# Kernel tuning notes

Hardware: AMD Instinct MI355X
Metric: run time of the kernel (lower is better)

The kernel has to match this reference:

```python
import jax, jax.numpy as jnp
import numpy as np

EPS = 1e-6      # l2_norm / denom clamp eps
BN_EPS = 1e-5   # BatchNorm eps


def _l2norm(x):
    # torch.norm(p=2, dim=-2, keepdim=True).clamp_min(eps)
    n = jnp.sqrt(jnp.sum(x * x, axis=-2, keepdims=True))
    return x / jnp.maximum(n, EPS)


def setup_inputs() -> dict:
    key = jax.random.key(0)
    ks = jax.random.split(key, 9)
    B, Cin_each, Co, H, W = 4, 256, 256, 128, 128
    Cq = Co // 8  # in_places // scale
    Cin = 4 * Cin_each
    return {
        "s5": jax.random.normal(ks[0], (B, Cin_each, H, W), jnp.float32),
        "s4": jax.random.normal(ks[1], (B, Cin_each, H, W), jnp.float32),
        "s3": jax.random.normal(ks[2], (B, Cin_each, H, W), jnp.float32),
        "s2": jax.random.normal(ks[3], (B, Cin_each, H, W), jnp.float32),
        # ConvBnRelu: 1x1 conv (no bias) + BN affine params
        "w_conv": jax.random.normal(ks[4], (Co, Cin), jnp.float32) * 0.03,
        "bn_gamma": jnp.ones((Co,), jnp.float32),
        "bn_beta": jnp.zeros((Co,), jnp.float32),
        # Attention 1x1 convs (with bias)
        "wq": jax.random.normal(ks[5], (Cq, Co), jnp.float32) * 0.06,
        "bq": jnp.zeros((Cq,), jnp.float32),
        "wk": jax.random.normal(ks[6], (Cq, Co), jnp.float32) * 0.06,
        "bk": jnp.zeros((Cq,), jnp.float32),
        "wv": jax.random.normal(ks[7], (Co, Co), jnp.float32) * 0.06,
        "bv": jnp.zeros((Co,), jnp.float32),
        # gamma is Parameter(zeros(1)) in the source; set nonzero so the
        # attention branch contributes to the output for kernel testing.
        "gamma": jnp.array(0.5, jnp.float32),
    }


def reference(s5, s4, s3, s2, w_conv, bn_gamma, bn_beta,
              wq, bq, wk, bk, wv, bv, gamma):
    # --- ConvBnRelu (1x1 conv, train-mode BN, ReLU) ---
    fcat = jnp.concatenate([s5, s4, s3, s2], axis=1)            # [B, 4C, H, W]
    x = jnp.einsum('oc,bchw->bohw', w_conv, fcat)               # 1x1 conv
    mu = x.mean(axis=(0, 2, 3), keepdims=True)
    var = x.var(axis=(0, 2, 3), keepdims=True)                  # biased, as torch BN
    x = (x - mu) / jnp.sqrt(var + BN_EPS)
    x = x * bn_gamma[None, :, None, None] + bn_beta[None, :, None, None]
    feat = jax.nn.relu(x)                                       # [B, C, H, W]

    # --- linear Attention (L2-norm QK, KV trick, no softmax) ---
    B, C, H, W = feat.shape
    N = H * W
    X = feat.reshape(B, C, N)
    Q = jnp.einsum('qc,bcn->bqn', wq, X) + bq[None, :, None]    # [B, Cq, N]
    K = jnp.einsum('qc,bcn->bqn', wk, X) + bk[None, :, None]    # [B, Cq, N]
    V = jnp.einsum('oc,bcn->bon', wv, X) + bv[None, :, None]    # [B, C, N]

    Qn = _l2norm(Q)                                             # norm over channel dim
    Kn = _l2norm(K)

    # denom: N + Q . sum_n K
    e = jnp.einsum('bqn,bq->bn', Qn, Kn.sum(axis=-1))           # [B, N]
    tailor = 1.0 / jnp.maximum(jnp.asarray(N, Qn.dtype) + e, 1e-6)

    # KV trick: [B, Cq, C] then project back through Q
    matrix = jnp.einsum('bqn,bcn->bqc', Kn, V)                  # [B, Cq, C]
    matrix_sum = V.sum(axis=-1)[:, :, None] + \
        jnp.einsum('bqn,bqc->bcn', Qn, matrix)                  # [B, C, N]

    weight_value = matrix_sum * tailor[:, None, :]              # [B, C, N]
    out = gamma * weight_value.reshape(B, C, H, W)
    out = jnp.nan_to_num(out, nan=0.0, posinf=1.0, neginf=-1.0)

    return out + feat
```

## Files before the change

### kernel.cpp

```cpp
#include <hip/hip_runtime.h>

#define B_   4
#define CO   256
#define CIN  1024
#define CQ   32
#define HN   16384
#define NPIX 65536
#define NTOT ((size_t)B_ * CO * HN)

typedef unsigned short ushort_t;
typedef __attribute__((ext_vector_type(8))) short bf16x8;
typedef __attribute__((ext_vector_type(4))) float f32x4;

__device__ __forceinline__ unsigned bf16pair(float x, float y) {
    unsigned xu = __float_as_uint(x), yu = __float_as_uint(y);
    unsigned xr = (xu + 0x7FFFu + ((xu >> 16) & 1u)) >> 16;
    unsigned yr = (yu + 0x7FFFu + ((yu >> 16) & 1u)) >> 16;
    return xr | (yr << 16);
}
__device__ __forceinline__ ushort_t bf16of(float x) {
    unsigned u = __float_as_uint(x);
    return (ushort_t)((u + 0x7FFFu + ((u >> 16) & 1u)) >> 16);
}
__device__ __forceinline__ float bf2f(ushort_t h) {
    return __uint_as_float(((unsigned)h) << 16);
}
__device__ __forceinline__ void unpack8(uint4 u, float* f) {
    f[0] = __uint_as_float(u.x << 16); f[1] = __uint_as_float(u.x & 0xffff0000u);
    f[2] = __uint_as_float(u.y << 16); f[3] = __uint_as_float(u.y & 0xffff0000u);
    f[4] = __uint_as_float(u.z << 16); f[5] = __uint_as_float(u.z & 0xffff0000u);
    f[6] = __uint_as_float(u.w << 16); f[7] = __uint_as_float(u.w & 0xffff0000u);
}
__device__ __forceinline__ void async16(void* lds, const void* g) {
    __builtin_amdgcn_global_load_lds(
        (const __attribute__((address_space(1))) void*)g,
        (__attribute__((address_space(3))) void*)lds, 16, 0, 0);
}

__global__ __launch_bounds__(256) void wcvt(
    const float* __restrict__ w, const float* __restrict__ wq,
    const float* __restrict__ wk, const float* __restrict__ wv,
    ushort_t* __restrict__ w_bf, ushort_t* __restrict__ wqk_bf,
    ushort_t* __restrict__ wv_bf)
{
    int i = blockIdx.x * 256 + threadIdx.x;
    if (i < 262144) {
        w_bf[i] = bf16of(w[i]);
    } else if (i < 278528) {
        int l = i - 262144; int row = l >> 8, col = l & 255;
        float v = (row < 32) ? wq[row * 256 + col] : wk[(row - 32) * 256 + col];
        wqk_bf[l] = bf16of(v);
    } else {
        int l = i - 278528;
        wv_bf[l] = bf16of(wv[l]);
    }
}

__global__ __launch_bounds__(256) void conv_mfma4(
    const float* __restrict__ s5, const float* __restrict__ s4,
    const float* __restrict__ s3, const float* __restrict__ s2,
    const ushort_t* __restrict__ w_bf, ushort_t* __restrict__ xb,
    float* __restrict__ accum)
{
    __shared__ ushort_t Aw[2][128 * 32];
    __shared__ ushort_t Bn[2][128 * 40];
    const int o0 = blockIdx.x * 128;
    const int n0 = blockIdx.y * 128;
    const int b  = blockIdx.z;
    const int tid = threadIdx.x;
    const int wave = tid >> 6, lane = tid & 63, l15 = lane & 15, quad = lane >> 4;
    const int wm = wave & 1, wn = wave >> 1;
    const int n_st = tid & 127;
    const int kqb  = tid >> 7;
    const int bswz = ((n_st >> 3) & 3) << 1;
    f32x4 acc[4][4] = {};
    float v[4][4];

    auto loadB = [&](int k0) {
        const float* base = (k0 < 256) ? s5 : (k0 < 512) ? s4
                          : (k0 < 768) ? s3 : s2;
        const float* sp = base + ((size_t)b * 256 + (k0 & 255)) * HN + n0 + n_st;
        #pragma unroll
        for (int i = 0; i < 4; ++i) {
            const float* cp = sp + (size_t)(kqb + 2 * i) * 4 * HN;
            #pragma unroll
            for (int j = 0; j < 4; ++j) v[i][j] = cp[(size_t)j * HN];
        }
    };
    auto storeB = [&](int bi) {
        ushort_t* Bp = Bn[bi];
        #pragma unroll
        for (int i = 0; i < 4; ++i) {
            int pos = (kqb + 2 * i) ^ bswz;
            uint2 u = make_uint2(bf16pair(v[i][0], v[i][1]),
                                 bf16pair(v[i][2], v[i][3]));
            *(uint2*)&Bp[n_st * 40 + pos * 4] = u;
        }
    };
    auto issueA = [&](int k0, int bi) {
        #pragma unroll
        for (int r = 0; r < 2; ++r) {
            int row  = r * 64 + wave * 16;
            int orow = row + (lane >> 2);
            const ushort_t* g = w_bf + (size_t)(o0 + orow) * CIN + k0
                                + (((lane & 3) ^ ((orow >> 1) & 3)) << 3);
            async16(&Aw[bi][row * 32], g);
        }
    };

    issueA(0, 0);
    loadB(0);

    int buf = 0;
    for (int k0 = 0; k0 < CIN; k0 += 32) {
        storeB(buf);
        asm volatile("s_waitcnt lgkmcnt(0)" ::: "memory");
        __builtin_amdgcn_s_barrier();
        __builtin_amdgcn_sched_barrier(0);
        if (k0 + 32 < CIN) { issueA(k0 + 32, buf ^ 1); loadB(k0 + 32); }
        bf16x8 af[4], bfv[4];
        #pragma unroll
        for (int tm = 0; tm < 4; ++tm) {
            int orow = wm * 64 + tm * 16 + l15;
            int pos  = quad ^ ((orow >> 1) & 3);
            af[tm] = *(const bf16x8*)&Aw[buf][orow * 32 + pos * 8];
        }
        #pragma unroll
        for (int tn = 0; tn < 4; ++tn) {
            int nl = wn * 64 + tn * 16 + l15;
            int p0 = (2 * quad) ^ (((nl >> 3) & 3) << 1);
            bfv[tn] = *(const bf16x8*)&Bn[buf][nl * 40 + p0 * 4];
        }
        #pragma unroll
        for (int tm = 0; tm < 4; ++tm)
            #pragma unroll
            for (int tn = 0; tn < 4; ++tn)
                acc[tm][tn] = __builtin_amdgcn_mfma_f32_16x16x32_bf16(
                    af[tm], bfv[tn], acc[tm][tn], 0, 0, 0);
        buf ^= 1;
    }

    #pragma unroll
    for (int tm = 0; tm < 4; ++tm)
        #pragma unroll
        for (int r = 0; r < 4; ++r) {
            float s = 0.f, ss = 0.f;
            #pragma unroll
            for (int tn = 0; tn < 4; ++tn) {
                float x = acc[tm][tn][r];
                s += x; ss += x * x;
            }
            s += __shfl_xor(s, 1); ss += __shfl_xor(ss, 1);
            s += __shfl_xor(s, 2); ss += __shfl_xor(ss, 2);
            s += __shfl_xor(s, 4); ss += __shfl_xor(ss, 4);
            s += __shfl_xor(s, 8); ss += __shfl_xor(ss, 8);
            if (l15 == 0) {
                int o = o0 + wm * 64 + tm * 16 + quad * 4 + r;
                atomicAdd(&accum[o], s);
                atomicAdd(&accum[256 + o], ss);
            }
        }

    ushort_t* st = Bn[0];
    const int orow = tid >> 3, oseg = tid & 7;
    #pragma unroll
    for (int tm = 0; tm < 4; ++tm) {
        if (tm) __syncthreads();
        #pragma unroll
        for (int r = 0; r < 4; ++r) {
            int row = wm * 16 + quad * 4 + r;
            #pragma unroll
            for (int tn = 0; tn < 4; ++tn)
                st[row * 136 + wn * 64 + tn * 16 + l15] = bf16of(acc[tm][tn][r]);
        }
        __syncthreads();
        {
            int c = o0 + (orow >> 4) * 64 + tm * 16 + (orow & 15);
            size_t base = ((size_t)(b * CO + c)) * HN + n0 + oseg * 16;
            const uint4* sp = (const uint4*)&st[orow * 136 + oseg * 16];
            *(uint4*)(xb + base)     = sp[0];
            *(uint4*)(xb + base + 8) = sp[1];
        }
    }
}

__global__ __launch_bounds__(256) void bn_finalize(
    const float* __restrict__ accum, const float* __restrict__ g,
    const float* __restrict__ bt, float* __restrict__ scale,
    float* __restrict__ shift)
{
    int o = threadIdx.x;
    float mu  = accum[o] / (float)NPIX;
    float var = accum[256 + o] / (float)NPIX - mu * mu;
    float sc  = g[o] * rsqrtf(var + 1e-5f);
    scale[o] = sc;
    shift[o] = bt[o] - mu * sc;
}

__global__ __launch_bounds__(256) void bnrelu_t(
    const ushort_t* __restrict__ xb, const float* __restrict__ scale,
    const float* __restrict__ shift, ushort_t* __restrict__ featT)
{
    __shared__ ushort_t sh[64 * 68];
    const int hn0 = blockIdx.x * 64, c0 = blockIdx.y * 64, b = blockIdx.z;
    const int tid = threadIdx.x;
    {
        int cl = tid >> 2, seg = tid & 3;
        float sc = scale[c0 + cl], sf = shift[c0 + cl];
        const ushort_t* src = xb + ((size_t)(b * CO + c0 + cl)) * HN + hn0 + seg * 16;
        #pragma unroll
        for (int h = 0; h < 2; ++h) {
            uint4 u = *(const uint4*)(src + h * 8);
            float f[8]; unpack8(u, f);
            #pragma unroll
            for (int j = 0; j < 8; ++j) {
                float v = fmaxf(fmaf(sc, f[j], sf), 0.f);
                sh[(seg * 16 + h * 8 + j) * 68 + cl] = bf16of(v);
            }
        }
    }
    __syncthreads();
    {
        int nl = tid >> 2, seg = tid & 3;
        size_t gn = (size_t)b * HN + hn0 + nl;
        ushort_t* dst = featT + gn * CO + c0 + seg * 16;
        #pragma unroll
        for (int j = 0; j < 4; ++j)
            *(uint2*)(dst + j * 4) = *(const uint2*)&sh[nl * 68 + seg * 16 + j * 4];
    }
}

__global__ __launch_bounds__(256) void qk_mfma(
    const ushort_t* __restrict__ featT, const ushort_t* __restrict__ wqk_bf,
    const float* __restrict__ bq, const float* __restrict__ bk,
    ushort_t* __restrict__ Qt, ushort_t* __restrict__ KtT,
    float* __restrict__ Ksum)
{
    __shared__ ushort_t At[128 * 32];
    __shared__ ushort_t Bt[64 * 32];
    const int n0 = blockIdx.x * 128;
    const int b  = n0 >> 14;
    const int hn0 = n0 & 16383;
    const int tid = threadIdx.x;
    const int wave = tid >> 6, lane = tid & 63, l15 = lane & 15, quad = lane >> 4;
    const int nsub = (wave & 1) * 64;
    const int isK  = wave >> 1;
    f32x4 acc[4][2] = {};

    for (int k0 = 0; k0 < CO; k0 += 32) {
        #pragma unroll
        for (int r = 0; r < 2; ++r) {
            int row = r * 64 + wave * 16;
            const ushort_t* g = featT + (size_t)(n0 + row + (lane >> 2)) * CO
                                + k0 + (lane & 3) * 8;
            async16(&At[row * 32], g);
        }
        {
            int row = wave * 16;
            const ushort_t* g = wqk_bf + (size_t)(row + (lane >> 2)) * CO
                                + k0 + (lane & 3) * 8;
            async16(&Bt[row * 32], g);
        }
        __syncthreads();
        bf16x8 af[4], bfv[2];
        #pragma unroll
        for (int tm = 0; tm < 4; ++tm)
            af[tm] = *(const bf16x8*)&At[(nsub + tm * 16 + l15) * 32 + quad * 8];
        #pragma unroll
        for (int tc = 0; tc < 2; ++tc)
            bfv[tc] = *(const bf16x8*)&Bt[(isK * 32 + tc * 16 + l15) * 32 + quad * 8];
        #pragma unroll
        for (int tm = 0; tm < 4; ++tm)
            #pragma unroll
            for (int tc = 0; tc < 2; ++tc)
                acc[tm][tc] = __builtin_amdgcn_mfma_f32_16x16x32_bf16(
                    af[tm], bfv[tc], acc[tm][tc], 0, 0, 0);
        __syncthreads();
    }
    const float bias0 = isK ? bk[l15]      : bq[l15];
    const float bias1 = isK ? bk[16 + l15] : bq[16 + l15];
    float ks0 = 0.f, ks1 = 0.f;
    #pragma unroll
    for (int tm = 0; tm < 4; ++tm)
        #pragma unroll
        for (int r = 0; r < 4; ++r) {
            float v0 = acc[tm][0][r] + bias0;
            float v1 = acc[tm][1][r] + bias1;
            float sq = v0 * v0 + v1 * v1;
            sq += __shfl_xor(sq, 1); sq += __shfl_xor(sq, 2);
            sq += __shfl_xor(sq, 4); sq += __shfl_xor(sq, 8);
            float inv = 1.f / fmaxf(sqrtf(sq), 1e-6f);
            v0 *= inv; v1 *= inv;
            if (isK) {
                int hn = hn0 + nsub + tm * 16 + quad * 4 + r;
                KtT[((size_t)(b * CQ + l15)) * HN + hn]      = bf16of(v0);
                KtT[((size_t)(b * CQ + 16 + l15)) * HN + hn] = bf16of(v1);
            } else {
                int n = n0 + nsub + tm * 16 + quad * 4 + r;
                Qt[(size_t)n * CQ + l15]      = bf16of(v0);
                Qt[(size_t)n * CQ + 16 + l15] = bf16of(v1);
            }
            ks0 += v0; ks1 += v1;
        }
    if (isK) {
        ks0 += __shfl_xor(ks0, 16); ks0 += __shfl_xor(ks0, 32);
        ks1 += __shfl_xor(ks1, 16); ks1 += __shfl_xor(ks1, 32);
        if (quad == 0) {
            atomicAdd(&Ksum[b * CQ + l15],      ks0);
            atomicAdd(&Ksum[b * CQ + 16 + l15], ks1);
        }
    }
}

__global__ __launch_bounds__(256) void v_kv_mfma(
    const ushort_t* __restrict__ featT, const ushort_t* __restrict__ wv_bf,
    const float* __restrict__ bv, const ushort_t* __restrict__ KtT,
    float* __restrict__ matT, float* __restrict__ Vsum)
{
    __shared__ ushort_t sh[128 * 136];
    ushort_t* At = sh;
    ushort_t* Bt = sh + 4096;
    const int n0  = blockIdx.x * 128;
    const int co0 = blockIdx.y * 128;
    const int b   = n0 >> 14;
    const int hn0 = n0 & 16383;
    const int tid = threadIdx.x;
    const int wave = tid >> 6, lane = tid & 63, l15 = lane & 15, quad = lane >> 4;
    const int wm = wave & 1, wn = wave >> 1;
    f32x4 acc[4][4] = {};

    for (int k0 = 0; k0 < CO; k0 += 32) {
        #pragma unroll
        for (int r = 0; r < 2; ++r) {
            int row = r * 64 + wave * 16;
            const ushort_t* ga = featT + (size_t)(n0 + row + (lane >> 2)) * CO
                                 + k0 + (lane & 3) * 8;
            async16(&At[row * 32], ga);
            const ushort_t* gb = wv_bf + (size_t)(co0 + row + (lane >> 2)) * CO
                                 + k0 + (lane & 3) * 8;
            async16(&Bt[row * 32], gb);
        }
        __syncthreads();
        bf16x8 af[4], bfv[4];
        #pragma unroll
        for (int tm = 0; tm < 4; ++tm)
            af[tm] = *(const bf16x8*)&At[(wm * 64 + tm * 16 + l15) * 32 + quad * 8];
        #pragma unroll
        for (int tn = 0; tn < 4; ++tn)
            bfv[tn] = *(const bf16x8*)&Bt[(wn * 64 + tn * 16 + l15) * 32 + quad * 8];
        #pragma unroll
        for (int tm = 0; tm < 4; ++tm)
            #pragma unroll
            for (int tn = 0; tn < 4; ++tn)
                acc[tm][tn] = __builtin_amdgcn_mfma_f32_16x16x32_bf16(
                    af[tm], bfv[tn], acc[tm][tn], 0, 0, 0);
        __syncthreads();
    }
    ushort_t* Vlds = sh;
    float bvl[4], vsum_p[4] = {};
    #pragma unroll
    for (int tn = 0; tn < 4; ++tn) bvl[tn] = bv[co0 + wn * 64 + tn * 16 + l15];
    #pragma unroll
    for (int tm = 0; tm < 4; ++tm)
        #pragma unroll
        for (int tn = 0; tn < 4; ++tn) {
            float x0 = acc[tm][tn][0] + bvl[tn];
            float x1 = acc[tm][tn][1] + bvl[tn];
            float x2 = acc[tm][tn][2] + bvl[tn];
            float x3 = acc[tm][tn][3] + bvl[tn];
            vsum_p[tn] += (x0 + x1) + (x2 + x3);
            uint2 u = make_uint2(bf16pair(x0, x1), bf16pair(x2, x3));
            int c_loc = wn * 64 + tn * 16 + l15;
            int nb    = wm * 64 + tm * 16 + quad * 4;
            *(uint2*)&Vlds[c_loc * 136 + nb] = u;
        }
    #pragma unroll
    for (int tn = 0; tn < 4; ++tn) {
        float s = vsum_p[tn];
        s += __shfl_xor(s, 16); s += __shfl_xor(s, 32);
        if (quad == 0)
            atomicAdd(&Vsum[b * CO + co0 + wn * 64 + tn * 16 + l15], s);
    }
    __syncthreads();
    f32x4 acc2[2][2] = {};
    #pragma unroll
    for (int ks = 0; ks < 4; ++ks) {
        bf16x8 a2[2], b2[2];
        #pragma unroll
        for (int t2 = 0; t2 < 2; ++t2)
            a2[t2] = *(const bf16x8*)&Vlds[(wave * 32 + t2 * 16 + l15) * 136
                                           + ks * 32 + quad * 8];
        #pragma unroll
        for (int tc = 0; tc < 2; ++tc)
            b2[tc] = *(const bf16x8*)&KtT[((size_t)(b * CQ + tc * 16 + l15)) * HN
                                          + hn0 + ks * 32 + quad * 8];
        #pragma unroll
        for (int t2 = 0; t2 < 2; ++t2)
            #pragma unroll
            for (int tc = 0; tc < 2; ++tc)
                acc2[t2][tc] = __builtin_amdgcn_mfma_f32_16x16x32_bf16(
                    a2[t2], b2[tc], acc2[t2][tc], 0, 0, 0);
    }
    #pragma unroll
    for (int t2 = 0; t2 < 2; ++t2)
        #pragma unroll
        for (int tc = 0; tc < 2; ++tc)
            #pragma unroll
            for (int r = 0; r < 4; ++r) {
                int c = co0 + wave * 32 + t2 * 16 + quad * 4 + r;
                atomicAdd(&matT[b * 8192 + c * CQ + tc * 16 + l15],
                          acc2[t2][tc][r]);
            }
}

__global__ __launch_bounds__(256) void tailor_k(
    const ushort_t* __restrict__ Qt, const float* __restrict__ Ksum,
    float* __restrict__ tailor)
{
    __shared__ float ks[CQ];
    const int n = blockIdx.x * 256 + threadIdx.x;
    const int b = n >> 14;
    if (threadIdx.x < CQ) ks[threadIdx.x] = Ksum[b * CQ + threadIdx.x];
    __syncthreads();
    const uint4* q = (const uint4*)&Qt[(size_t)n * CQ];
    float e = 0.f;
    #pragma unroll
    for (int i = 0; i < 4; ++i) {
        float f[8]; unpack8(q[i], f);
        #pragma unroll
        for (int j = 0; j < 8; ++j) e += f[j] * ks[i * 8 + j];
    }
    tailor[n] = 1.f / fmaxf((float)HN + e, 1e-6f);
}

__global__ __launch_bounds__(256) void final_mfma(
    const ushort_t* __restrict__ xb, const ushort_t* __restrict__ Qt,
    const float* __restrict__ matT, const float* __restrict__ Vsum,
    const float* __restrict__ tailor, const float* __restrict__ scale,
    const float* __restrict__ shift, const float* __restrict__ gamma_p,
    float* __restrict__ out)
{
    __shared__ float sh[32 * 132];
    const int c0 = blockIdx.x * 128;
    const int n0 = blockIdx.y * 128;
    const int b  = n0 >> 14, hn0 = n0 & 16383;
    const int tid = threadIdx.x;
    const int wave = tid >> 6, lane = tid & 63, l15 = lane & 15, quad = lane >> 4;
    const int wm = wave & 1, wn = wave >> 1;
    const float gamma = gamma_p[0];

    bf16x8 af[4], bfv[4];
    #pragma unroll
    for (int tm = 0; tm < 4; ++tm) {
        int c = c0 + wm * 64 + tm * 16 + l15;
        const float* mp = matT + b * 8192 + c * CQ + quad * 8;
        float4 m0 = *(const float4*)mp;
        float4 m1 = *(const float4*)(mp + 4);
        union { bf16x8 v; unsigned u[4]; } t;
        t.u[0] = bf16pair(m0.x, m0.y); t.u[1] = bf16pair(m0.z, m0.w);
        t.u[2] = bf16pair(m1.x, m1.y); t.u[3] = bf16pair(m1.z, m1.w);
        af[tm] = t.v;
    }
    #pragma unroll
    for (int tn = 0; tn < 4; ++tn) {
        int n = n0 + wn * 64 + tn * 16 + l15;
        bfv[tn] = *(const bf16x8*)&Qt[(size_t)n * CQ + quad * 8];
    }
    f32x4 acc[4][4] = {};
    #pragma unroll
    for (int tm = 0; tm < 4; ++tm)
        #pragma unroll
        for (int tn = 0; tn < 4; ++tn)
            acc[tm][tn] = __builtin_amdgcn_mfma_f32_16x16x32_bf16(
                af[tm], bfv[tn], acc[tm][tn], 0, 0, 0);

    float tl[4];
    #pragma unroll
    for (int tn = 0; tn < 4; ++tn) tl[tn] = tailor[n0 + wn * 64 + tn * 16 + l15];

    const int orow = tid >> 3, oseg = tid & 7;
    #pragma unroll
    for (int tm = 0; tm < 4; ++tm) {
        if (tm) __syncthreads();
        #pragma unroll
        for (int r = 0; r < 4; ++r) {
            int c = c0 + wm * 64 + tm * 16 + quad * 4 + r;
            float vs = Vsum[b * CO + c];
            int row = wm * 16 + quad * 4 + r;
            #pragma unroll
            for (int tn = 0; tn < 4; ++tn) {
                float val = gamma * (acc[tm][tn][r] + vs) * tl[tn];
                if (isnan(val)) val = 0.f;
                else if (isinf(val)) val = (val > 0.f) ? 1.f : -1.f;
                sh[row * 132 + wn * 64 + tn * 16 + l15] = val;
            }
        }
        __syncthreads();
        {
            int c = c0 + (orow >> 4) * 64 + tm * 16 + (orow & 15);
            float sc = scale[c], sf = shift[c];
            size_t base = ((size_t)(b * CO + c)) * HN + hn0 + oseg * 16;
            const float* sp = &sh[orow * 132 + oseg * 16];
            const uint4* xp = (const uint4*)(xb + base);
            #pragma unroll
            for (int h = 0; h < 2; ++h) {
                uint4 u = xp[h];
                float f[8]; unpack8(u, f);
                float4 q0, q1;
                q0.x = sp[h * 8 + 0] + fmaxf(fmaf(sc, f[0], sf), 0.f);
                q0.y = sp[h * 8 + 1] + fmaxf(fmaf(sc, f[1], sf), 0.f);
                q0.z = sp[h * 8 + 2] + fmaxf(fmaf(sc, f[2], sf), 0.f);
                q0.w = sp[h * 8 + 3] + fmaxf(fmaf(sc, f[3], sf), 0.f);
                q1.x = sp[h * 8 + 4] + fmaxf(fmaf(sc, f[4], sf), 0.f);
                q1.y = sp[h * 8 + 5] + fmaxf(fmaf(sc, f[5], sf), 0.f);
                q1.z = sp[h * 8 + 6] + fmaxf(fmaf(sc, f[6], sf), 0.f);
                q1.w = sp[h * 8 + 7] + fmaxf(fmaf(sc, f[7], sf), 0.f);
                *(float4*)(out + base + h * 8)     = q0;
                *(float4*)(out + base + h * 8 + 4) = q1;
            }
        }
    }
}

extern "C" void kernel_launch(void* const* d_in, const int* in_sizes, int n_in,
                              void* d_out, int out_size, void* d_ws, size_t ws_size,
                              hipStream_t stream)
{
    const float* s5      = (const float*)d_in[0];
    const float* s4      = (const float*)d_in[1];
    const float* s3      = (const float*)d_in[2];
    const float* s2      = (const float*)d_in[3];
    const float* w_conv  = (const float*)d_in[4];
    const float* bn_g    = (const float*)d_in[5];
    const float* bn_b    = (const float*)d_in[6];
    const float* wq      = (const float*)d_in[7];
    const float* bq      = (const float*)d_in[8];
    const float* wk      = (const float*)d_in[9];
    const float* bk      = (const float*)d_in[10];
    const float* wv      = (const float*)d_in[11];
    const float* bv      = (const float*)d_in[12];
    const float* gamma_p = (const float*)d_in[13];

    char* p = (char*)d_ws;
    ushort_t* xb     = (ushort_t*)p;  p += NTOT * 2;
    ushort_t* featT  = (ushort_t*)p;  p += NTOT * 2;
    ushort_t* Qt     = (ushort_t*)p;  p += (size_t)NPIX * CQ * 2;
    ushort_t* KtT    = (ushort_t*)p;  p += (size_t)NPIX * CQ * 2;
    ushort_t* w_bf   = (ushort_t*)p;  p += (size_t)CO * CIN * 2;
    ushort_t* wqk_bf = (ushort_t*)p;  p += 64 * CO * 2;
    ushort_t* wv_bf  = (ushort_t*)p;  p += (size_t)CO * CO * 2;
    float* matT  = (float*)p;
    float* Ksum  = matT + (size_t)B_ * CO * CQ;
    float* Vsum  = Ksum + B_ * CQ;
    float* accum = Vsum + B_ * CO;
    size_t zero_bytes = (size_t)(32768 + 128 + 1024 + 512) * 4;
    p += zero_bytes;
    float* scale  = (float*)p;  p += 256 * 4;
    float* shift  = (float*)p;  p += 256 * 4;
    float* tailor = (float*)p;  p += (size_t)NPIX * 4;

    hipMemsetAsync(matT, 0, zero_bytes, stream);
    wcvt<<<1344, 256, 0, stream>>>(w_conv, wq, wk, wv, w_bf, wqk_bf, wv_bf);
    conv_mfma4<<<dim3(2, 128, B_), 256, 0, stream>>>(s5, s4, s3, s2, w_bf, xb,
                                                     accum);
    bn_finalize<<<1, 256, 0, stream>>>(accum, bn_g, bn_b, scale, shift);
    bnrelu_t<<<dim3(256, 4, B_), 256, 0, stream>>>(xb, scale, shift, featT);
    qk_mfma<<<512, 256, 0, stream>>>(featT, wqk_bf, bq, bk, Qt, KtT, Ksum);
    tailor_k<<<256, 256, 0, stream>>>(Qt, Ksum, tailor);
    v_kv_mfma<<<dim3(512, 2), 256, 0, stream>>>(featT, wv_bf, bv, KtT, matT, Vsum);
    final_mfma<<<dim3(2, 512), 256, 0, stream>>>(xb, Qt, matT, Vsum, tailor,
                                                 scale, shift, gamma_p,
                                                 (float*)d_out);
}
```

Before: 479.9 us.

## Deepen conv GEMM B-operand prefetch to two register stages

```diff
diff --git a/kernel.cpp b/kernel.cpp
--- a/kernel.cpp
+++ b/kernel.cpp
@@ -56,7 +56,7 @@
     }
 }
 
-__global__ __launch_bounds__(256) void conv_mfma4(
+__global__ __launch_bounds__(256) void conv_mfma5(
     const float* __restrict__ s5, const float* __restrict__ s4,
     const float* __restrict__ s3, const float* __restrict__ s2,
     const ushort_t* __restrict__ w_bf, ushort_t* __restrict__ xb,
@@ -74,9 +74,10 @@
     const int kqb  = tid >> 7;
     const int bswz = ((n_st >> 3) & 3) << 1;
     f32x4 acc[4][4] = {};
-    float v[4][4];
-
-    auto loadB = [&](int k0) {
+    float vA[4][4], vB[4][4];
+
+    auto loadB = [&](float (&v)[4][4], int t) {
+        const int k0 = t << 5;
         const float* base = (k0 < 256) ? s5 : (k0 < 512) ? s4
                           : (k0 < 768) ? s3 : s2;
         const float* sp = base + ((size_t)b * 256 + (k0 & 255)) * HN + n0 + n_st;
@@ -87,7 +88,7 @@
             for (int j = 0; j < 4; ++j) v[i][j] = cp[(size_t)j * HN];
         }
     };
-    auto storeB = [&](int bi) {
+    auto storeB = [&](float (&v)[4][4], int bi) {
         ushort_t* Bp = Bn[bi];
         #pragma unroll
         for (int i = 0; i < 4; ++i) {
@@ -97,7 +98,8 @@
             *(uint2*)&Bp[n_st * 40 + pos * 4] = u;
         }
     };
-    auto issueA = [&](int k0, int bi) {
+    auto issueA = [&](int t, int bi) {
+        const int k0 = t << 5;
         #pragma unroll
         for (int r = 0; r < 2; ++r) {
             int row  = r * 64 + wave * 16;
@@ -107,29 +109,19 @@
             async16(&Aw[bi][row * 32], g);
         }
     };
-
-    issueA(0, 0);
-    loadB(0);
-
-    int buf = 0;
-    for (int k0 = 0; k0 < CIN; k0 += 32) {
-        storeB(buf);
-        asm volatile("s_waitcnt lgkmcnt(0)" ::: "memory");
-        __builtin_amdgcn_s_barrier();
-        __builtin_amdgcn_sched_barrier(0);
-        if (k0 + 32 < CIN) { issueA(k0 + 32, buf ^ 1); loadB(k0 + 32); }
+    auto compute = [&](int bi) {
         bf16x8 af[4], bfv[4];
         #pragma unroll
         for (int tm = 0; tm < 4; ++tm) {
             int orow = wm * 64 + tm * 16 + l15;
             int pos  = quad ^ ((orow >> 1) & 3);
-            af[tm] = *(const bf16x8*)&Aw[buf][orow * 32 + pos * 8];
+            af[tm] = *(const bf16x8*)&Aw[bi][orow * 32 + pos * 8];
         }
         #pragma unroll
         for (int tn = 0; tn < 4; ++tn) {
             int nl = wn * 64 + tn * 16 + l15;
             int p0 = (2 * quad) ^ (((nl >> 3) & 3) << 1);
-            bfv[tn] = *(const bf16x8*)&Bn[buf][nl * 40 + p0 * 4];
+            bfv[tn] = *(const bf16x8*)&Bn[bi][nl * 40 + p0 * 4];
         }
         #pragma unroll
         for (int tm = 0; tm < 4; ++tm)
@@ -137,7 +129,38 @@
             for (int tn = 0; tn < 4; ++tn)
                 acc[tm][tn] = __builtin_amdgcn_mfma_f32_16x16x32_bf16(
                     af[tm], bfv[tn], acc[tm][tn], 0, 0, 0);
-        buf ^= 1;
+    };
+
+    issueA(0, 0);
+    __builtin_amdgcn_sched_barrier(0);
+    loadB(vA, 0);
+    __builtin_amdgcn_sched_barrier(0);
+    loadB(vB, 1);
+    __builtin_amdgcn_sched_barrier(0);
+    storeB(vA, 0);
+    asm volatile("s_waitcnt vmcnt(16) lgkmcnt(0)" ::: "memory");
+    __builtin_amdgcn_s_barrier();
+    __builtin_amdgcn_sched_barrier(0);
+
+    for (int t = 0; t < 32; t += 2) {
+        issueA((t + 1 < 32) ? t + 1 : 31, 1);
+        __builtin_amdgcn_sched_barrier(0);
+        loadB(vA, (t + 2 < 32) ? t + 2 : 31);
+        __builtin_amdgcn_sched_barrier(0);
+        compute(0);
+        storeB(vB, 1);
+        asm volatile("s_waitcnt vmcnt(16) lgkmcnt(0)" ::: "memory");
+        __builtin_amdgcn_s_barrier();
+        __builtin_amdgcn_sched_barrier(0);
+        issueA((t + 2 < 32) ? t + 2 : 31, 0);
+        __builtin_amdgcn_sched_barrier(0);
+        loadB(vB, (t + 3 < 32) ? t + 3 : 31);
+        __builtin_amdgcn_sched_barrier(0);
+        compute(1);
+        storeB(vA, 0);
+        asm volatile("s_waitcnt vmcnt(16) lgkmcnt(0)" ::: "memory");
+        __builtin_amdgcn_s_barrier();
+        __builtin_amdgcn_sched_barrier(0);
     }
 
     #pragma unroll
@@ -165,7 +188,7 @@
     const int orow = tid >> 3, oseg = tid & 7;
     #pragma unroll
     for (int tm = 0; tm < 4; ++tm) {
-        if (tm) __syncthreads();
+        __syncthreads();
         #pragma unroll
         for (int r = 0; r < 4; ++r) {
             int row = wm * 16 + quad * 4 + r;
@@ -561,7 +584,7 @@
 
     hipMemsetAsync(matT, 0, zero_bytes, stream);
     wcvt<<<1344, 256, 0, stream>>>(w_conv, wq, wk, wv, w_bf, wqk_bf, wv_bf);
-    conv_mfma4<<<dim3(2, 128, B_), 256, 0, stream>>>(s5, s4, s3, s2, w_bf, xb,
+    conv_mfma5<<<dim3(2, 128, B_), 256, 0, stream>>>(s5, s4, s3, s2, w_bf, xb,
                                                      accum);
     bn_finalize<<<1, 256, 0, stream>>>(accum, bn_g, bn_b, scale, shift);
     bnrelu_t<<<dim3(256, 4, B_), 256, 0, stream>>>(xb, scale, shift, featT);
```

Measured after the change: 482.7 us. No clear change (+0.6%).
